# Kernel optimization log

Measured on AMD Instinct MI355X. Metric: run time of the kernel, lower is better.

## Reference

```python
import jax, jax.numpy as jnp
import numpy as np

N_EMBD = 1024
N_HEAD = 16
LN_EPS = 1e-5

def setup_inputs() -> dict:
    key = jax.random.key(0)
    ks = jax.random.split(key, 12)
    B, T, C = 2, 2048, N_EMBD
    s = lambda k, shape, scale=0.02: (jax.random.normal(k, shape, dtype=jnp.float32) * scale)
    return {
        "x": jax.random.normal(ks[0], (B, T, C), dtype=jnp.float32),
        "ln1_g": jnp.ones((C,), jnp.float32),
        "ln1_b": jnp.zeros((C,), jnp.float32),
        "W_attn": s(ks[1], (C, 3 * C)),
        "b_attn": jnp.zeros((3 * C,), jnp.float32),
        "W_o": s(ks[2], (C, C)),
        "b_o": jnp.zeros((C,), jnp.float32),
        "ln2_g": jnp.ones((C,), jnp.float32),
        "ln2_b": jnp.zeros((C,), jnp.float32),
        "W_fc": s(ks[3], (C, 4 * C)),
        "b_fc": jnp.zeros((4 * C,), jnp.float32),
        "W_fc2": s(ks[4], (4 * C, C)),
        "b_fc2": jnp.zeros((C,), jnp.float32),
    }

def _layernorm(x, g, b):
    mu = jnp.mean(x, axis=-1, keepdims=True)
    var = jnp.mean(jnp.square(x - mu), axis=-1, keepdims=True)
    return (x - mu) * jax.lax.rsqrt(var + LN_EPS) * g + b

def reference(x, ln1_g, ln1_b, W_attn, b_attn, W_o, b_o, ln2_g, ln2_b, W_fc, b_fc, W_fc2, b_fc2):
    B, T, C = x.shape
    H, D = N_HEAD, C // N_HEAD
    # ---- attention branch (use_cache=False: T_total == T, causal mask) ----
    h = _layernorm(x, ln1_g, ln1_b)
    qkv = h @ W_attn + b_attn                       # [B,T,3C]
    q, k, v = jnp.split(qkv, 3, axis=-1)
    q = q.reshape(B, T, H, D).transpose(0, 2, 1, 3)  # [B,H,T,D]
    k = k.reshape(B, T, H, D).transpose(0, 2, 1, 3)
    v = v.reshape(B, T, H, D).transpose(0, 2, 1, 3)
    w = jnp.einsum('bhqd,bhkd->bhqk', q, k) / jnp.sqrt(jnp.float32(D))  # [B,H,T,T]
    causal = jnp.tril(jnp.ones((T, T), dtype=bool))
    w = jnp.where(causal, w, jnp.float32(-jnp.inf))
    w = jax.nn.softmax(w, axis=-1)
    y = jnp.einsum('bhqk,bhkd->bhqd', w, v)          # [B,H,T,D]
    y = y.transpose(0, 2, 1, 3).reshape(B, T, C)
    x = x + (y @ W_o + b_o)
    # ---- MLP branch ----
    h2 = _layernorm(x, ln2_g, ln2_b)
    h2 = jax.nn.gelu(h2 @ W_fc + b_fc, approximate=True)  # tanh approx, matches nn.GELU('tanh')
    x = x + (h2 @ W_fc2 + b_fc2)
    return x
```

## Files before the change

kernel.cpp:

```cpp
#include <hip/hip_runtime.h>


typedef unsigned short u16;
typedef unsigned int u32;
typedef __attribute__((ext_vector_type(8))) short v8s;
typedef __attribute__((ext_vector_type(4))) float v4f;

#define GAS __attribute__((address_space(1)))
#define LAS __attribute__((address_space(3)))

__device__ __forceinline__ u16 f2bf(float f) {
  u32 u = __float_as_uint(f);
  u = (u + 0x7FFF + ((u >> 16) & 1)) >> 16;
  return (u16)u;
}
__device__ __forceinline__ float bf2f(u16 h) {
  return __uint_as_float(((u32)h) << 16);
}
__device__ __forceinline__ float fast_tanh(float x) {
  return 1.f - 2.f / (1.f + __expf(2.f * x));
}

__global__ __launch_bounds__(256)
void wtrans(const float* __restrict__ W, u16* __restrict__ Wt, int K, int N) {
  __shared__ float tile[32][33];
  const int n0 = blockIdx.x << 5, k0 = blockIdx.y << 5;
  const int r = threadIdx.x >> 5, c = threadIdx.x & 31;
#pragma unroll
  for (int i = 0; i < 4; ++i)
    tile[r + 8 * i][c] = W[(size_t)(k0 + r + 8 * i) * N + n0 + c];
  __syncthreads();
#pragma unroll
  for (int i = 0; i < 4; ++i)
    Wt[(size_t)(n0 + r + 8 * i) * K + k0 + c] = f2bf(tile[c][r + 8 * i]);
}

__global__ __launch_bounds__(256)
void ln_bf16(const float* __restrict__ x, const float* __restrict__ g,
             const float* __restrict__ be, u16* __restrict__ out) {
  constexpr int C = 1024;
  const int row = blockIdx.x, t = threadIdx.x;
  const float4 v = ((const float4*)(x + (size_t)row * C))[t];
  float s = v.x + v.y + v.z + v.w;
#pragma unroll
  for (int m = 32; m >= 1; m >>= 1) s += __shfl_xor(s, m);
  __shared__ float red[4], red2[4];
  if ((t & 63) == 0) red[t >> 6] = s;
  __syncthreads();
  const float mu = (red[0] + red[1] + red[2] + red[3]) * (1.f / C);
  const float dx = v.x - mu, dy = v.y - mu, dz = v.z - mu, dw = v.w - mu;
  float s2 = dx * dx + dy * dy + dz * dz + dw * dw;
#pragma unroll
  for (int m = 32; m >= 1; m >>= 1) s2 += __shfl_xor(s2, m);
  if ((t & 63) == 0) red2[t >> 6] = s2;
  __syncthreads();
  const float var = (red2[0] + red2[1] + red2[2] + red2[3]) * (1.f / C);
  const float rs = rsqrtf(var + 1e-5f);
  const int c = t << 2;
  u16 o0 = f2bf(dx * rs * g[c + 0] + be[c + 0]);
  u16 o1 = f2bf(dy * rs * g[c + 1] + be[c + 1]);
  u16 o2 = f2bf(dz * rs * g[c + 2] + be[c + 2]);
  u16 o3 = f2bf(dw * rs * g[c + 3] + be[c + 3]);
  uint2 pk;
  pk.x = (u32)o0 | ((u32)o1 << 16);
  pk.y = (u32)o2 | ((u32)o3 << 16);
  *(uint2*)(out + (size_t)row * C + c) = pk;
}

template <int EPI>
__global__ __launch_bounds__(256)
void gemm_bt(const u16* __restrict__ A, const u16* __restrict__ Bt,
             const float* __restrict__ bias, const float* __restrict__ res,
             void* __restrict__ outp, int M, int N, int K) {
  __shared__ u16 As[128 * 32];
  __shared__ u16 Bs[128 * 32];
  const int tid = threadIdx.x;
  const int wave = tid >> 6, lane = tid & 63;
  const int m0 = blockIdx.y << 7, n0 = blockIdx.x << 7;

  v4f acc[4][4];
  const v4f vz = {0.f, 0.f, 0.f, 0.f};
#pragma unroll
  for (int i = 0; i < 4; ++i)
#pragma unroll
    for (int j = 0; j < 4; ++j) acc[i][j] = vz;

  const int wm = (wave >> 1) << 6, wn = (wave & 1) << 6;
  const int sr = lane >> 2;
  const int sc = (lane & 3) << 3;
  const int fr = lane & 15;
  const int fk = (lane >> 4) << 3;
  const int c0 = wave << 1;

  u16* lA0 = As + (c0 + 0) * 512;
  u16* lA1 = As + (c0 + 1) * 512;
  u16* lB0 = Bs + (c0 + 0) * 512;
  u16* lB1 = Bs + (c0 + 1) * 512;
  const u16* gA0 = A + (size_t)(m0 + c0 * 16 + sr) * K + sc;
  const u16* gA1 = A + (size_t)(m0 + c0 * 16 + 16 + sr) * K + sc;
  const u16* gB0 = Bt + (size_t)(n0 + c0 * 16 + sr) * K + sc;
  const u16* gB1 = Bt + (size_t)(n0 + c0 * 16 + 16 + sr) * K + sc;

  for (int k0 = 0; k0 < K; k0 += 32) {
    __builtin_amdgcn_global_load_lds((GAS const u32*)(gA0 + k0), (LAS u32*)lA0, 16, 0, 0);
    __builtin_amdgcn_global_load_lds((GAS const u32*)(gA1 + k0), (LAS u32*)lA1, 16, 0, 0);
    __builtin_amdgcn_global_load_lds((GAS const u32*)(gB0 + k0), (LAS u32*)lB0, 16, 0, 0);
    __builtin_amdgcn_global_load_lds((GAS const u32*)(gB1 + k0), (LAS u32*)lB1, 16, 0, 0);
    __syncthreads();
    v8s af[4], bfr[4];
#pragma unroll
    for (int mi = 0; mi < 4; ++mi)
      af[mi] = *(const v8s*)&As[(wm + mi * 16 + fr) * 32 + fk];
#pragma unroll
    for (int ni = 0; ni < 4; ++ni)
      bfr[ni] = *(const v8s*)&Bs[(wn + ni * 16 + fr) * 32 + fk];
#pragma unroll
    for (int mi = 0; mi < 4; ++mi)
#pragma unroll
      for (int ni = 0; ni < 4; ++ni)
        acc[mi][ni] = __builtin_amdgcn_mfma_f32_16x16x32_bf16(af[mi], bfr[ni], acc[mi][ni], 0, 0, 0);
    __syncthreads();
  }

  const int er = (lane >> 4) << 2;
#pragma unroll
  for (int mi = 0; mi < 4; ++mi) {
#pragma unroll
    for (int ni = 0; ni < 4; ++ni) {
      const int col = n0 + wn + ni * 16 + fr;
      const float bcol = bias[col];
#pragma unroll
      for (int r = 0; r < 4; ++r) {
        const int row = m0 + wm + mi * 16 + er + r;
        float v = acc[mi][ni][r] + bcol;
        if constexpr (EPI == 1) {
          const float t = fast_tanh(0.7978845608028654f * (v + 0.044715f * v * v * v));
          v = 0.5f * v * (1.f + t);
        }
        if constexpr (EPI == 2) {
          v += res[(size_t)row * N + col];
          ((float*)outp)[(size_t)row * N + col] = v;
        } else {
          ((u16*)outp)[(size_t)row * N + col] = f2bf(v);
        }
      }
    }
  }
}

template <int EPI>
__global__ __launch_bounds__(256)
void gemm_bt_n64(const u16* __restrict__ A, const u16* __restrict__ Bt,
                 const float* __restrict__ bias, const float* __restrict__ res,
                 void* __restrict__ outp, int M, int N, int K) {
  __shared__ u16 As[4][128 * 32];
  __shared__ u16 Bs[4][64 * 32];
  const int tid = threadIdx.x;
  const int wave = tid >> 6, lane = tid & 63;
  const int m0 = blockIdx.y << 7, n0 = blockIdx.x << 6;

  v4f acc[4][2];
  const v4f vz = {0.f, 0.f, 0.f, 0.f};
#pragma unroll
  for (int i = 0; i < 4; ++i)
#pragma unroll
    for (int j = 0; j < 2; ++j) acc[i][j] = vz;

  const int wm = (wave >> 1) << 6, wn = (wave & 1) << 5;
  const int sr = lane >> 2;
  const int sc = (lane & 3) << 3;
  const int fr = lane & 15;
  const int fk = (lane >> 4) << 3;

  const u16* gA0 = A + (size_t)(m0 + wave * 32 + sr) * K + sc;
  const u16* gA1 = A + (size_t)(m0 + wave * 32 + 16 + sr) * K + sc;
  const u16* gB0 = Bt + (size_t)(n0 + wave * 16 + sr) * K + sc;
  const int aoff = wave * 1024;
  const int boff = wave * 512;

  const u32 asb = (u32)(size_t)(LAS const u16*)&As[0][0];
  const u32 bsb = (u32)(size_t)(LAS const u16*)&Bs[0][0];
  const u32 afrag = (u32)(((wm + fr) << 6) + (fk << 1));
  const u32 bfrag = (u32)(((wn + fr) << 6) + (fk << 1));

  const int nk = K >> 5;

#define N64_ISSUE(t, bf)                                                      \
  do {                                                                        \
    const int k0_ = (t) << 5;                                                 \
    __builtin_amdgcn_global_load_lds((GAS const u32*)(gA0 + k0_),             \
                                     (LAS u32*)(As[bf] + aoff), 16, 0, 0);    \
    __builtin_amdgcn_global_load_lds((GAS const u32*)(gA1 + k0_),             \
                                     (LAS u32*)(As[bf] + aoff + 512), 16, 0, 0); \
    __builtin_amdgcn_global_load_lds((GAS const u32*)(gB0 + k0_),             \
                                     (LAS u32*)(Bs[bf] + boff), 16, 0, 0);    \
  } while (0)

  N64_ISSUE(0, 0);
  N64_ISSUE(1, 1);
  N64_ISSUE(2, 2);

  auto compute = [&](int kt) __attribute__((always_inline)) {
    const u32 ab = asb + ((u32)(kt & 3) << 13) + afrag;
    const u32 bb = bsb + ((u32)(kt & 3) << 12) + bfrag;
    v8s a0, a1, a2, a3, b0, b1;
    asm volatile("ds_read_b128 %0, %1 offset:0"    : "=v"(a0) : "v"(ab));
    asm volatile("ds_read_b128 %0, %1 offset:1024" : "=v"(a1) : "v"(ab));
    asm volatile("ds_read_b128 %0, %1 offset:2048" : "=v"(a2) : "v"(ab));
    asm volatile("ds_read_b128 %0, %1 offset:3072" : "=v"(a3) : "v"(ab));
    asm volatile("ds_read_b128 %0, %1 offset:0"    : "=v"(b0) : "v"(bb));
    asm volatile("ds_read_b128 %0, %1 offset:1024" : "=v"(b1) : "v"(bb));
    asm volatile("s_waitcnt lgkmcnt(0)"
                 : "+v"(a0), "+v"(a1), "+v"(a2), "+v"(a3), "+v"(b0), "+v"(b1)
                 :
                 : "memory");
    acc[0][0] = __builtin_amdgcn_mfma_f32_16x16x32_bf16(a0, b0, acc[0][0], 0, 0, 0);
    acc[0][1] = __builtin_amdgcn_mfma_f32_16x16x32_bf16(a0, b1, acc[0][1], 0, 0, 0);
    acc[1][0] = __builtin_amdgcn_mfma_f32_16x16x32_bf16(a1, b0, acc[1][0], 0, 0, 0);
    acc[1][1] = __builtin_amdgcn_mfma_f32_16x16x32_bf16(a1, b1, acc[1][1], 0, 0, 0);
    acc[2][0] = __builtin_amdgcn_mfma_f32_16x16x32_bf16(a2, b0, acc[2][0], 0, 0, 0);
    acc[2][1] = __builtin_amdgcn_mfma_f32_16x16x32_bf16(a2, b1, acc[2][1], 0, 0, 0);
    acc[3][0] = __builtin_amdgcn_mfma_f32_16x16x32_bf16(a3, b0, acc[3][0], 0, 0, 0);
    acc[3][1] = __builtin_amdgcn_mfma_f32_16x16x32_bf16(a3, b1, acc[3][1], 0, 0, 0);
  };

  for (int kt = 0; kt < nk - 2; ++kt) {
    asm volatile("s_waitcnt vmcnt(6)" ::: "memory");
    __builtin_amdgcn_s_barrier();
    if (kt + 3 < nk) N64_ISSUE(kt + 3, (kt + 3) & 3);
    compute(kt);
  }
  asm volatile("s_waitcnt vmcnt(3)" ::: "memory");
  __builtin_amdgcn_s_barrier();
  compute(nk - 2);
  asm volatile("s_waitcnt vmcnt(0)" ::: "memory");
  __builtin_amdgcn_s_barrier();
  compute(nk - 1);
#undef N64_ISSUE

  const int er = (lane >> 4) << 2;
#pragma unroll
  for (int mi = 0; mi < 4; ++mi) {
#pragma unroll
    for (int ni = 0; ni < 2; ++ni) {
      const int col = n0 + wn + ni * 16 + fr;
      const float bcol = bias[col];
#pragma unroll
      for (int r = 0; r < 4; ++r) {
        const int row = m0 + wm + mi * 16 + er + r;
        float v = acc[mi][ni][r] + bcol;
        if constexpr (EPI == 1) {
          const float t = fast_tanh(0.7978845608028654f * (v + 0.044715f * v * v * v));
          v = 0.5f * v * (1.f + t);
        }
        if constexpr (EPI == 2) {
          v += res[(size_t)row * N + col];
          ((float*)outp)[(size_t)row * N + col] = v;
        } else {
          ((u16*)outp)[(size_t)row * N + col] = f2bf(v);
        }
      }
    }
  }
}

__global__ __launch_bounds__(256)
void transpose_v(const u16* __restrict__ qkv, u16* __restrict__ Vt) {
  __shared__ u16 tile[64][65];
  const int t0 = blockIdx.x << 6;
  const int bh = blockIdx.y;
  const int b = bh >> 4, h = bh & 15;
  const int r4 = threadIdx.x >> 6, c = threadIdx.x & 63;
#pragma unroll
  for (int i = 0; i < 16; ++i) {
    const int r = r4 * 16 + i;
    tile[r][c] = qkv[(size_t)(b * 2048 + t0 + r) * 3072 + 2048 + h * 64 + c];
  }
  __syncthreads();
#pragma unroll
  for (int i = 0; i < 16; ++i) {
    const int d = r4 * 16 + i;
    Vt[(size_t)bh * 64 * 2048 + (size_t)d * 2048 + t0 + c] = tile[c][d];
  }
}

constexpr int PSTR = 88;

template <bool MASKED>
__device__ __forceinline__ void attn_sub(
    const v8s (&kf)[4][2], const v8s (&vfr)[4][2], const v8s (&qf)[2],
    v4f (&ot)[4], float& m_i, float& l_i, u16* __restrict__ pw,
    const int kb, const int qrow, const int fr, const int fg) {
  const v4f vz = {0.f, 0.f, 0.f, 0.f};
  v4f st[4];
#pragma unroll
  for (int ks = 0; ks < 4; ++ks) {
    st[ks] = vz;
    st[ks] = __builtin_amdgcn_mfma_f32_16x16x32_bf16(kf[ks][0], qf[0], st[ks], 0, 0, 0);
    st[ks] = __builtin_amdgcn_mfma_f32_16x16x32_bf16(kf[ks][1], qf[1], st[ks], 0, 0, 0);
  }
  const int q = qrow + fr;
  float e[4][4];
  float mt = -1e30f;
#pragma unroll
  for (int ks = 0; ks < 4; ++ks)
#pragma unroll
    for (int r = 0; r < 4; ++r) {
      float v = st[ks][r] * 0.125f;
      if (MASKED) v = (kb + ks * 16 + fg * 4 + r <= q) ? v : -1e30f;
      e[ks][r] = v;
      mt = fmaxf(mt, v);
    }
  mt = fmaxf(mt, __shfl_xor(mt, 16));
  mt = fmaxf(mt, __shfl_xor(mt, 32));
  const float m_new = fmaxf(m_i, mt);
  const float alpha = __expf(m_i - m_new);
  m_i = m_new;
  float ls = 0.f;
#pragma unroll
  for (int ks = 0; ks < 4; ++ks)
#pragma unroll
    for (int r = 0; r < 4; ++r) {
      e[ks][r] = __expf(e[ks][r] - m_new);
      ls += e[ks][r];
    }
  ls += __shfl_xor(ls, 16);
  ls += __shfl_xor(ls, 32);
  l_i = l_i * alpha + ls;
#pragma unroll
  for (int ds = 0; ds < 4; ++ds) ot[ds] *= alpha;
#pragma unroll
  for (int ks = 0; ks < 4; ++ks) {
    ushort4 pk4;
    pk4.x = f2bf(e[ks][0]);
    pk4.y = f2bf(e[ks][1]);
    pk4.z = f2bf(e[ks][2]);
    pk4.w = f2bf(e[ks][3]);
    *(ushort4*)&pw[fr * PSTR + ks * 16 + fg * 4] = pk4;
  }
  const v8s pf0 = *(const v8s*)&pw[fr * PSTR + fg * 8];
  const v8s pf1 = *(const v8s*)&pw[fr * PSTR + 32 + fg * 8];
#pragma unroll
  for (int ds = 0; ds < 4; ++ds) {
    ot[ds] = __builtin_amdgcn_mfma_f32_16x16x32_bf16(vfr[ds][0], pf0, ot[ds], 0, 0, 0);
    ot[ds] = __builtin_amdgcn_mfma_f32_16x16x32_bf16(vfr[ds][1], pf1, ot[ds], 0, 0, 0);
  }
}

__global__ __launch_bounds__(256)
void attn_kernel(const u16* __restrict__ qkv, const u16* __restrict__ Vt,
                 u16* __restrict__ y) {
  constexpr int T = 2048, D = 64, C = 1024, QS = 3072;
  __shared__ alignas(16) u16 Ktile[2][64 * 64];
  __shared__ alignas(16) u16 Vtile[2][64 * 64];
  __shared__ alignas(16) u16 Pw[4][16 * PSTR];

  const int tid = threadIdx.x, wave = tid >> 6, lane = tid & 63;
  const int fr = lane & 15, fg = lane >> 4;
  const int bh = blockIdx.y, b = bh >> 4, h = bh & 15;
  const int ta = blockIdx.x, tb = 31 - ta;
  const u16* qkvb = qkv + (size_t)b * T * QS + h * 64;
  const u16* Kg = qkvb + 1024;
  const u16* Vh = Vt + (size_t)bh * D * T;
  u16* pw = &Pw[wave][0];

  const int rowA = ta * 64 + wave * 16;
  const int rowB = tb * 64 + wave * 16;

  v8s qfA[2], qfB[2];
#pragma unroll
  for (int dh = 0; dh < 2; ++dh) {
    qfA[dh] = *(const v8s*)&qkvb[(size_t)(rowA + fr) * QS + dh * 32 + fg * 8];
    qfB[dh] = *(const v8s*)&qkvb[(size_t)(rowB + fr) * QS + dh * 32 + fg * 8];
  }

  const v4f vz = {0.f, 0.f, 0.f, 0.f};
  v4f otA[4], otB[4];
#pragma unroll
  for (int ds = 0; ds < 4; ++ds) { otA[ds] = vz; otB[ds] = vz; }
  float mA = -1e30f, lA = 0.f, mB = -1e30f, lB = 0.f;

  const int srow = lane >> 3;
  const int sg0 = lane & 7;

  const int nt = tb + 1;
  {
#pragma unroll
    for (int cc = 0; cc < 2; ++cc) {
      const int r0 = wave * 16 + cc * 8;
      const int rr = r0 + srow;
      const int gg = sg0 ^ (rr & 7);
      __builtin_amdgcn_global_load_lds(
          (GAS const u32*)(Kg + (size_t)rr * QS + gg * 8),
          (LAS u32*)(Ktile[0] + r0 * 64), 16, 0, 0);
      __builtin_amdgcn_global_load_lds(
          (GAS const u32*)(Vh + (size_t)rr * T + gg * 8),
          (LAS u32*)(Vtile[0] + r0 * 64), 16, 0, 0);
    }
  }
  for (int kt = 0; kt < nt; ++kt) {
    __syncthreads();
    if (kt + 1 < nt) {
      const int kb1 = (kt + 1) << 6;
      const int nb = (kt + 1) & 1;
#pragma unroll
      for (int cc = 0; cc < 2; ++cc) {
        const int r0 = wave * 16 + cc * 8;
        const int rr = r0 + srow;
        const int gg = sg0 ^ (rr & 7);
        __builtin_amdgcn_global_load_lds(
            (GAS const u32*)(Kg + (size_t)(kb1 + rr) * QS + gg * 8),
            (LAS u32*)(Ktile[nb] + r0 * 64), 16, 0, 0);
        __builtin_amdgcn_global_load_lds(
            (GAS const u32*)(Vh + (size_t)rr * T + kb1 + gg * 8),
            (LAS u32*)(Vtile[nb] + r0 * 64), 16, 0, 0);
      }
    }
    const u16* Kt = Ktile[kt & 1];
    const u16* Vi = Vtile[kt & 1];
    const int kb = kt << 6;
    const int swz = fr & 7;
    v8s kf[4][2], vfr[4][2];
#pragma unroll
    for (int ks = 0; ks < 4; ++ks) {
      const int rr = ks * 16 + fr;
      kf[ks][0] = *(const v8s*)&Kt[rr * 64 + ((0 + fg) ^ swz) * 8];
      kf[ks][1] = *(const v8s*)&Kt[rr * 64 + ((4 + fg) ^ swz) * 8];
      vfr[ks][0] = *(const v8s*)&Vi[rr * 64 + ((0 + fg) ^ swz) * 8];
      vfr[ks][1] = *(const v8s*)&Vi[rr * 64 + ((4 + fg) ^ swz) * 8];
    }
    if (kt < ta) {
      attn_sub<false>(kf, vfr, qfA, otA, mA, lA, pw, kb, rowA, fr, fg);
      attn_sub<false>(kf, vfr, qfB, otB, mB, lB, pw, kb, rowB, fr, fg);
    } else if (kt == ta) {
      attn_sub<true>(kf, vfr, qfA, otA, mA, lA, pw, kb, rowA, fr, fg);
      attn_sub<false>(kf, vfr, qfB, otB, mB, lB, pw, kb, rowB, fr, fg);
    } else if (kt < tb) {
      attn_sub<false>(kf, vfr, qfB, otB, mB, lB, pw, kb, rowB, fr, fg);
    } else {
      attn_sub<true>(kf, vfr, qfB, otB, mB, lB, pw, kb, rowB, fr, fg);
    }
  }

  const float invA = 1.f / lA, invB = 1.f / lB;
#pragma unroll
  for (int ds = 0; ds < 4; ++ds) {
    ushort4 a4, b4;
    a4.x = f2bf(otA[ds][0] * invA);
    a4.y = f2bf(otA[ds][1] * invA);
    a4.z = f2bf(otA[ds][2] * invA);
    a4.w = f2bf(otA[ds][3] * invA);
    b4.x = f2bf(otB[ds][0] * invB);
    b4.y = f2bf(otB[ds][1] * invB);
    b4.z = f2bf(otB[ds][2] * invB);
    b4.w = f2bf(otB[ds][3] * invB);
    *(ushort4*)&y[(size_t)(b * T + rowA + fr) * C + h * D + ds * 16 + fg * 4] = a4;
    *(ushort4*)&y[(size_t)(b * T + rowB + fr) * C + h * D + ds * 16 + fg * 4] = b4;
  }
}

extern "C" void kernel_launch(void* const* d_in, const int* in_sizes, int n_in,
                              void* d_out, int out_size, void* d_ws, size_t ws_size,
                              hipStream_t stream) {
  const float* x      = (const float*)d_in[0];
  const float* ln1_g  = (const float*)d_in[1];
  const float* ln1_b  = (const float*)d_in[2];
  const float* W_attn = (const float*)d_in[3];
  const float* b_attn = (const float*)d_in[4];
  const float* W_o    = (const float*)d_in[5];
  const float* b_o    = (const float*)d_in[6];
  const float* ln2_g  = (const float*)d_in[7];
  const float* ln2_b  = (const float*)d_in[8];
  const float* W_fc   = (const float*)d_in[9];
  const float* b_fc   = (const float*)d_in[10];
  const float* W_fc2  = (const float*)d_in[11];
  const float* b_fc2  = (const float*)d_in[12];
  float* out = (float*)d_out;
  char* ws = (char*)d_ws;

  const size_t MB = 1u << 20;
  u16* Wattn_t = (u16*)(ws + 0 * MB);
  u16* Wo_t    = (u16*)(ws + 6 * MB);
  u16* Wfc_t   = (u16*)(ws + 8 * MB);
  u16* Wfc2_t  = (u16*)(ws + 16 * MB);
  float* x1    = (float*)(ws + 24 * MB);
  u16* h1      = (u16*)(ws + 40 * MB);
  u16* qkv     = (u16*)(ws + 48 * MB);
  u16* Vt      = (u16*)(ws + 88 * MB);
  u16* yb      = (u16*)(ws + 40 * MB);
  u16* h2      = (u16*)(ws + 48 * MB);
  u16* ab      = (u16*)(ws + 56 * MB);

  wtrans<<<dim3(3072 / 32, 1024 / 32), 256, 0, stream>>>(W_attn, Wattn_t, 1024, 3072);
  wtrans<<<dim3(1024 / 32, 1024 / 32), 256, 0, stream>>>(W_o, Wo_t, 1024, 1024);
  wtrans<<<dim3(4096 / 32, 1024 / 32), 256, 0, stream>>>(W_fc, Wfc_t, 1024, 4096);
  wtrans<<<dim3(1024 / 32, 4096 / 32), 256, 0, stream>>>(W_fc2, Wfc2_t, 4096, 1024);

  ln_bf16<<<4096, 256, 0, stream>>>(x, ln1_g, ln1_b, h1);
  gemm_bt<0><<<dim3(3072 / 128, 4096 / 128), 256, 0, stream>>>(
      h1, Wattn_t, b_attn, nullptr, qkv, 4096, 3072, 1024);
  transpose_v<<<dim3(2048 / 64, 32), 256, 0, stream>>>(qkv, Vt);
  attn_kernel<<<dim3(16, 32), 256, 0, stream>>>(qkv, Vt, yb);
  gemm_bt_n64<2><<<dim3(1024 / 64, 4096 / 128), 256, 0, stream>>>(
      yb, Wo_t, b_o, x, x1, 4096, 1024, 1024);
  ln_bf16<<<4096, 256, 0, stream>>>(x1, ln2_g, ln2_b, h2);
  gemm_bt<1><<<dim3(4096 / 128, 4096 / 128), 256, 0, stream>>>(
      h2, Wfc_t, b_fc, nullptr, ab, 4096, 4096, 1024);
  gemm_bt_n64<2><<<dim3(1024 / 64, 4096 / 128), 256, 0, stream>>>(
      ab, Wfc2_t, b_fc2, x1, out, 4096, 1024, 4096);
}
```

Baseline: 373.3 us.

## Multi-buffer LDS in 128x128 GEMM with three-stage async prefetch

Replaces the single-buffered GEMM loop with a 4-slot LDS ring buffer, keeping three k-tiles of global_load_lds in flight and using vmcnt waits plus a single barrier per iteration. Fragment reads are written as inline-asm ds_read_b128 with immediate offsets. The aim is to hide global memory latency behind the MFMA work and to drop the second barrier each iteration. In exchange the kernel uses 4x the LDS (64KB), which can lower occupancy, and hand-written waitcnt sequences are fragile.

```diff
diff --git a/kernel.cpp b/kernel.cpp
--- a/kernel.cpp
+++ b/kernel.cpp
@@ -69,11 +69,11 @@
 
 template <int EPI>
 __global__ __launch_bounds__(256)
-void gemm_bt(const u16* __restrict__ A, const u16* __restrict__ Bt,
-             const float* __restrict__ bias, const float* __restrict__ res,
-             void* __restrict__ outp, int M, int N, int K) {
-  __shared__ u16 As[128 * 32];
-  __shared__ u16 Bs[128 * 32];
+void gemm_bt_p(const u16* __restrict__ A, const u16* __restrict__ Bt,
+               const float* __restrict__ bias, const float* __restrict__ res,
+               void* __restrict__ outp, int M, int N, int K) {
+  __shared__ u16 As[4][128 * 32];
+  __shared__ u16 Bs[4][128 * 32];
   const int tid = threadIdx.x;
   const int wave = tid >> 6, lane = tid & 63;
   const int m0 = blockIdx.y << 7, n0 = blockIdx.x << 7;
@@ -92,35 +92,87 @@
   const int fk = (lane >> 4) << 3;
   const int c0 = wave << 1;
 
-  u16* lA0 = As + (c0 + 0) * 512;
-  u16* lA1 = As + (c0 + 1) * 512;
-  u16* lB0 = Bs + (c0 + 0) * 512;
-  u16* lB1 = Bs + (c0 + 1) * 512;
   const u16* gA0 = A + (size_t)(m0 + c0 * 16 + sr) * K + sc;
   const u16* gA1 = A + (size_t)(m0 + c0 * 16 + 16 + sr) * K + sc;
   const u16* gB0 = Bt + (size_t)(n0 + c0 * 16 + sr) * K + sc;
   const u16* gB1 = Bt + (size_t)(n0 + c0 * 16 + 16 + sr) * K + sc;
-
-  for (int k0 = 0; k0 < K; k0 += 32) {
-    __builtin_amdgcn_global_load_lds((GAS const u32*)(gA0 + k0), (LAS u32*)lA0, 16, 0, 0);
-    __builtin_amdgcn_global_load_lds((GAS const u32*)(gA1 + k0), (LAS u32*)lA1, 16, 0, 0);
-    __builtin_amdgcn_global_load_lds((GAS const u32*)(gB0 + k0), (LAS u32*)lB0, 16, 0, 0);
-    __builtin_amdgcn_global_load_lds((GAS const u32*)(gB1 + k0), (LAS u32*)lB1, 16, 0, 0);
-    __syncthreads();
-    v8s af[4], bfr[4];
-#pragma unroll
-    for (int mi = 0; mi < 4; ++mi)
-      af[mi] = *(const v8s*)&As[(wm + mi * 16 + fr) * 32 + fk];
-#pragma unroll
-    for (int ni = 0; ni < 4; ++ni)
-      bfr[ni] = *(const v8s*)&Bs[(wn + ni * 16 + fr) * 32 + fk];
-#pragma unroll
-    for (int mi = 0; mi < 4; ++mi)
-#pragma unroll
-      for (int ni = 0; ni < 4; ++ni)
-        acc[mi][ni] = __builtin_amdgcn_mfma_f32_16x16x32_bf16(af[mi], bfr[ni], acc[mi][ni], 0, 0, 0);
-    __syncthreads();
-  }
+  const int aoff = c0 * 512;
+
+  const u32 asb = (u32)(size_t)(LAS const u16*)&As[0][0];
+  const u32 bsb = (u32)(size_t)(LAS const u16*)&Bs[0][0];
+  const u32 afrag = (u32)(((wm + fr) << 6) + (fk << 1));
+  const u32 bfrag = (u32)(((wn + fr) << 6) + (fk << 1));
+
+  const int nk = K >> 5;
+
+#define P128_ISSUE(t, bf)                                                        \
+  do {                                                                           \
+    const int k0_ = (t) << 5;                                                    \
+    __builtin_amdgcn_global_load_lds((GAS const u32*)(gA0 + k0_),                \
+                                     (LAS u32*)(As[bf] + aoff), 16, 0, 0);       \
+    __builtin_amdgcn_global_load_lds((GAS const u32*)(gA1 + k0_),                \
+                                     (LAS u32*)(As[bf] + aoff + 512), 16, 0, 0); \
+    __builtin_amdgcn_global_load_lds((GAS const u32*)(gB0 + k0_),                \
+                                     (LAS u32*)(Bs[bf] + aoff), 16, 0, 0);       \
+    __builtin_amdgcn_global_load_lds((GAS const u32*)(gB1 + k0_),                \
+                                     (LAS u32*)(Bs[bf] + aoff + 512), 16, 0, 0); \
+  } while (0)
+
+  P128_ISSUE(0, 0);
+  P128_ISSUE(1, 1);
+  P128_ISSUE(2, 2);
+
+  auto compute = [&](int kt) __attribute__((always_inline)) {
+    const u32 ab = asb + ((u32)(kt & 3) << 13) + afrag;
+    const u32 bb = bsb + ((u32)(kt & 3) << 13) + bfrag;
+    v8s a0, a1, a2, a3, b0, b1, b2, b3;
+    asm volatile("ds_read_b128 %0, %1 offset:0"    : "=v"(a0) : "v"(ab));
+    asm volatile("ds_read_b128 %0, %1 offset:1024" : "=v"(a1) : "v"(ab));
+    asm volatile("ds_read_b128 %0, %1 offset:2048" : "=v"(a2) : "v"(ab));
+    asm volatile("ds_read_b128 %0, %1 offset:3072" : "=v"(a3) : "v"(ab));
+    asm volatile("ds_read_b128 %0, %1 offset:0"    : "=v"(b0) : "v"(bb));
+    asm volatile("ds_read_b128 %0, %1 offset:1024" : "=v"(b1) : "v"(bb));
+    asm volatile("ds_read_b128 %0, %1 offset:2048" : "=v"(b2) : "v"(bb));
+    asm volatile("ds_read_b128 %0, %1 offset:3072" : "=v"(b3) : "v"(bb));
+    asm volatile("s_waitcnt lgkmcnt(0)"
+                 : "+v"(a0), "+v"(a1), "+v"(a2), "+v"(a3),
+                   "+v"(b0), "+v"(b1), "+v"(b2), "+v"(b3)
+                 :
+                 : "memory");
+    acc[0][0] = __builtin_amdgcn_mfma_f32_16x16x32_bf16(a0, b0, acc[0][0], 0, 0, 0);
+    acc[0][1] = __builtin_amdgcn_mfma_f32_16x16x32_bf16(a0, b1, acc[0][1], 0, 0, 0);
+    acc[0][2] = __builtin_amdgcn_mfma_f32_16x16x32_bf16(a0, b2, acc[0][2], 0, 0, 0);
+    acc[0][3] = __builtin_amdgcn_mfma_f32_16x16x32_bf16(a0, b3, acc[0][3], 0, 0, 0);
+    acc[1][0] = __builtin_amdgcn_mfma_f32_16x16x32_bf16(a1, b0, acc[1][0], 0, 0, 0);
+    acc[1][1] = __builtin_amdgcn_mfma_f32_16x16x32_bf16(a1, b1, acc[1][1], 0, 0, 0);
+    acc[1][2] = __builtin_amdgcn_mfma_f32_16x16x32_bf16(a1, b2, acc[1][2], 0, 0, 0);
+    acc[1][3] = __builtin_amdgcn_mfma_f32_16x16x32_bf16(a1, b3, acc[1][3], 0, 0, 0);
+    acc[2][0] = __builtin_amdgcn_mfma_f32_16x16x32_bf16(a2, b0, acc[2][0], 0, 0, 0);
+    acc[2][1] = __builtin_amdgcn_mfma_f32_16x16x32_bf16(a2, b1, acc[2][1], 0, 0, 0);
+    acc[2][2] = __builtin_amdgcn_mfma_f32_16x16x32_bf16(a2, b2, acc[2][2], 0, 0, 0);
+    acc[2][3] = __builtin_amdgcn_mfma_f32_16x16x32_bf16(a2, b3, acc[2][3], 0, 0, 0);
+    acc[3][0] = __builtin_amdgcn_mfma_f32_16x16x32_bf16(a3, b0, acc[3][0], 0, 0, 0);
+    acc[3][1] = __builtin_amdgcn_mfma_f32_16x16x32_bf16(a3, b1, acc[3][1], 0, 0, 0);
+    acc[3][2] = __builtin_amdgcn_mfma_f32_16x16x32_bf16(a3, b2, acc[3][2], 0, 0, 0);
+    acc[3][3] = __builtin_amdgcn_mfma_f32_16x16x32_bf16(a3, b3, acc[3][3], 0, 0, 0);
+  };
+
+  for (int kt = 0; kt < nk - 3; ++kt) {
+    asm volatile("s_waitcnt vmcnt(8)" ::: "memory");
+    __builtin_amdgcn_s_barrier();
+    P128_ISSUE(kt + 3, (kt + 3) & 3);
+    compute(kt);
+  }
+  asm volatile("s_waitcnt vmcnt(8)" ::: "memory");
+  __builtin_amdgcn_s_barrier();
+  compute(nk - 3);
+  asm volatile("s_waitcnt vmcnt(4)" ::: "memory");
+  __builtin_amdgcn_s_barrier();
+  compute(nk - 2);
+  asm volatile("s_waitcnt vmcnt(0)" ::: "memory");
+  __builtin_amdgcn_s_barrier();
+  compute(nk - 1);
+#undef P128_ISSUE
 
   const int er = (lane >> 4) << 2;
 #pragma unroll
@@ -497,14 +549,14 @@
   wtrans<<<dim3(1024 / 32, 4096 / 32), 256, 0, stream>>>(W_fc2, Wfc2_t, 4096, 1024);
 
   ln_bf16<<<4096, 256, 0, stream>>>(x, ln1_g, ln1_b, h1);
-  gemm_bt<0><<<dim3(3072 / 128, 4096 / 128), 256, 0, stream>>>(
+  gemm_bt_p<0><<<dim3(3072 / 128, 4096 / 128), 256, 0, stream>>>(
       h1, Wattn_t, b_attn, nullptr, qkv, 4096, 3072, 1024);
   transpose_v<<<dim3(2048 / 64, 32), 256, 0, stream>>>(qkv, Vt);
   attn_kernel<<<dim3(16, 32), 256, 0, stream>>>(qkv, Vt, yb);
   gemm_bt_n64<2><<<dim3(1024 / 64, 4096 / 128), 256, 0, stream>>>(
       yb, Wo_t, b_o, x, x1, 4096, 1024, 1024);
   ln_bf16<<<4096, 256, 0, stream>>>(x1, ln2_g, ln2_b, h2);
-  gemm_bt<1><<<dim3(4096 / 128, 4096 / 128), 256, 0, stream>>>(
+  gemm_bt_p<1><<<dim3(4096 / 128, 4096 / 128), 256, 0, stream>>>(
       h2, Wfc_t, b_fc, nullptr, ab, 4096, 4096, 1024);
   gemm_bt_n64<2><<<dim3(1024 / 64, 4096 / 128), 256, 0, stream>>>(
       ab, Wfc2_t, b_fc2, x1, out, 4096, 1024, 4096);
```

New measurement: 364.8 us. 2.3% less time.
